# Kernel tuning notes

Measured on AMD Instinct MI355X. Metric: run time of the kernel, lower is better.

## Reference

```python
import jax, jax.numpy as jnp
import numpy as np

KS = 21        # kernel_size
SIGMA = 5.0    # sigma
C = 3          # channels
PAD = KS // 2  # reflection pad = 10


def _gaussian_kernel():
    # Matches torch construction: 2D isotropic Gaussian on integer grid, then
    # normalized to sum 1. Separable => outer product of 1D Gaussians.
    coords = jnp.arange(KS, dtype=jnp.float32)
    mean = (KS - 1) / 2.0
    g1 = jnp.exp(-((coords - mean) ** 2) / (2.0 * SIGMA ** 2))
    k2 = jnp.outer(g1, g1)
    k2 = k2 / jnp.sum(k2)
    # depthwise weight [C, 1, KS, KS] (OIHW with feature_group_count=C)
    return jnp.tile(k2[None, None, :, :], (C, 1, 1, 1))


def setup_inputs() -> dict:
    key = jax.random.key(0)
    x = jax.random.normal(key, (32, 3, 512, 512), dtype=jnp.float32)
    return {"x": x}


def reference(x):
    w = _gaussian_kernel()
    xp = jnp.pad(x, ((0, 0), (0, 0), (PAD, PAD), (PAD, PAD)), mode="reflect")
    out = jax.lax.conv_general_dilated(
        xp, w,
        window_strides=(1, 1),
        padding="VALID",
        dimension_numbers=("NCHW", "OIHW", "NCHW"),
        feature_group_count=C,
    )
    return out  # [B, C, H, W], same spatial size as input
```

## Files before the change

kernel.cpp:

```cpp
#include <hip/hip_runtime.h>
#include <math.h>


#define KS    21
#define PAD   10
#define TILE  64
#define LW    (TILE + 2 * PAD)
#define SKEW  2
#define LWX   88
#define SH    68
#define IMG_H 512
#define IMG_W 512
#define NT    256

__global__ __launch_bounds__(NT) void gauss_blur_kernel(
    const float* __restrict__ in, float* __restrict__ out)
{
    __shared__ __align__(16) float s_in[LW * LWX];
    __shared__ __align__(16) float s_h [LW * SH];

    float w[KS];
    {
        float s = 0.f;
#pragma unroll
        for (int k = 0; k < KS; ++k) {
            float d = (float)(k - PAD);
            w[k] = expf(-d * d * (1.0f / 50.0f));
            s += w[k];
        }
        float inv = 1.0f / s;
#pragma unroll
        for (int k = 0; k < KS; ++k) w[k] *= inv;
    }

    const int tid   = threadIdx.x;
    const int plane = blockIdx.z;
    const int x0    = blockIdx.x * TILE;
    const int y0    = blockIdx.y * TILE;
    const int xbase = x0 - PAD - SKEW;

    const float* __restrict__ pin = in + (size_t)plane * (IMG_H * IMG_W);

    if (xbase >= 0 && xbase + LWX <= IMG_W) {
        for (int idx = tid; idx < LW * (LWX / 4); idx += NT) {
            int ly = idx / (LWX / 4);
            int q  = idx - ly * (LWX / 4);
            int gy = y0 + ly - PAD;
            gy = (gy < 0) ? -gy : ((gy >= IMG_H) ? (2 * IMG_H - 2 - gy) : gy);
            float4 v = *(const float4*)&pin[gy * IMG_W + xbase + 4 * q];
            *(float4*)&s_in[ly * LWX + 4 * q] = v;
        }
    } else {
        for (int idx = tid; idx < LW * LWX; idx += NT) {
            int ly = idx / LWX;
            int j  = idx - ly * LWX;
            int gy = y0 + ly - PAD;
            int gx = xbase + j;
            gy = (gy < 0) ? -gy : ((gy >= IMG_H) ? (2 * IMG_H - 2 - gy) : gy);
            gx = (gx < 0) ? -gx : ((gx >= IMG_W) ? (2 * IMG_W - 2 - gx) : gx);
            s_in[idx] = pin[gy * IMG_W + gx];
        }
    }
    __syncthreads();

    for (int idx = tid; idx < LW * (TILE / 4); idx += NT) {
        int ly = idx >> 4;
        int lx = (idx & 15) << 2;
        const float4* rp = (const float4*)&s_in[ly * LWX + lx];
        float v[28];
#pragma unroll
        for (int t = 0; t < 7; ++t) {
            float4 f = rp[t];
            v[4 * t + 0] = f.x; v[4 * t + 1] = f.y;
            v[4 * t + 2] = f.z; v[4 * t + 3] = f.w;
        }
        float a0 = 0.f, a1 = 0.f, a2 = 0.f, a3 = 0.f;
#pragma unroll
        for (int k = 0; k < KS; ++k) {
            float wk = w[k];
            a0 += wk * v[k + 2];
            a1 += wk * v[k + 3];
            a2 += wk * v[k + 4];
            a3 += wk * v[k + 5];
        }
        *(float4*)&s_h[ly * SH + lx] = make_float4(a0, a1, a2, a3);
    }
    __syncthreads();

    {
        const int c  = tid & 63;
        const int rb = (tid >> 6) << 4;

        float acc[16];
#pragma unroll
        for (int r = 0; r < 16; ++r) acc[r] = 0.f;

#pragma unroll
        for (int t = 0; t < KS + 15; ++t) {
            float v = s_h[(rb + t) * SH + c];
#pragma unroll
            for (int r = 0; r < 16; ++r) {
                int k = t - r;
                if (k >= 0 && k < KS) acc[r] += w[k] * v;
            }
        }

        float* __restrict__ pout = out + (size_t)plane * (IMG_H * IMG_W)
                                       + (size_t)(y0 + rb) * IMG_W + (x0 + c);
#pragma unroll
        for (int r = 0; r < 16; ++r) pout[r * IMG_W] = acc[r];
    }
}

extern "C" void kernel_launch(void* const* d_in, const int* in_sizes, int n_in,
                              void* d_out, int out_size, void* d_ws, size_t ws_size,
                              hipStream_t stream)
{
    const float* x = (const float*)d_in[0];
    float* out = (float*)d_out;

    dim3 grid(IMG_W / TILE, IMG_H / TILE, 96);
    dim3 block(NT);
    gauss_blur_kernel<<<grid, block, 0, stream>>>(x, out);
}
```

Baseline: 226.0 us.

## Read input rows directly from global memory in horizontal pass, drop input LDS tile

Removes the shared-memory staging of the input tile and its barrier. The horizontal pass now loads its 28-element window straight from global memory with float4 reads, falling back to scalar reflected loads on edge tiles. It also adds a min-blocks-per-CU hint of 6 to the launch bounds. Together these cut LDS use and should allow more resident blocks, at the cost of overlapping global reads (seven float4s per thread with heavy overlap), which must now be served by the caches.

```diff
diff --git a/kernel.cpp b/kernel.cpp
--- a/kernel.cpp
+++ b/kernel.cpp
@@ -7,17 +7,15 @@
 #define TILE  64
 #define LW    (TILE + 2 * PAD)
 #define SKEW  2
-#define LWX   88
 #define SH    68
 #define IMG_H 512
 #define IMG_W 512
 #define NT    256
 
-__global__ __launch_bounds__(NT) void gauss_blur_kernel(
+__global__ __launch_bounds__(NT, 6) void gauss_blur_kernel(
     const float* __restrict__ in, float* __restrict__ out)
 {
-    __shared__ __align__(16) float s_in[LW * LWX];
-    __shared__ __align__(16) float s_h [LW * SH];
+    __shared__ __align__(16) float s_h[LW * SH];
 
     float w[KS];
     {
@@ -41,39 +39,34 @@
 
     const float* __restrict__ pin = in + (size_t)plane * (IMG_H * IMG_W);
 
-    if (xbase >= 0 && xbase + LWX <= IMG_W) {
-        for (int idx = tid; idx < LW * (LWX / 4); idx += NT) {
-            int ly = idx / (LWX / 4);
-            int q  = idx - ly * (LWX / 4);
-            int gy = y0 + ly - PAD;
-            gy = (gy < 0) ? -gy : ((gy >= IMG_H) ? (2 * IMG_H - 2 - gy) : gy);
-            float4 v = *(const float4*)&pin[gy * IMG_W + xbase + 4 * q];
-            *(float4*)&s_in[ly * LWX + 4 * q] = v;
-        }
-    } else {
-        for (int idx = tid; idx < LW * LWX; idx += NT) {
-            int ly = idx / LWX;
-            int j  = idx - ly * LWX;
-            int gy = y0 + ly - PAD;
-            int gx = xbase + j;
-            gy = (gy < 0) ? -gy : ((gy >= IMG_H) ? (2 * IMG_H - 2 - gy) : gy);
-            gx = (gx < 0) ? -gx : ((gx >= IMG_W) ? (2 * IMG_W - 2 - gx) : gx);
-            s_in[idx] = pin[gy * IMG_W + gx];
-        }
-    }
-    __syncthreads();
+    const bool xint = (xbase >= 0) && (xbase + 88 <= IMG_W);
 
     for (int idx = tid; idx < LW * (TILE / 4); idx += NT) {
         int ly = idx >> 4;
         int lx = (idx & 15) << 2;
-        const float4* rp = (const float4*)&s_in[ly * LWX + lx];
+        int gy = y0 + ly - PAD;
+        gy = (gy < 0) ? -gy : ((gy >= IMG_H) ? (2 * IMG_H - 2 - gy) : gy);
+        const float* __restrict__ rowp = pin + (size_t)gy * IMG_W;
+
         float v[28];
+        if (xint) {
+            const float4* rp = (const float4*)(rowp + xbase + lx);
 #pragma unroll
-        for (int t = 0; t < 7; ++t) {
-            float4 f = rp[t];
-            v[4 * t + 0] = f.x; v[4 * t + 1] = f.y;
-            v[4 * t + 2] = f.z; v[4 * t + 3] = f.w;
+            for (int t = 0; t < 7; ++t) {
+                float4 f = rp[t];
+                v[4 * t + 0] = f.x; v[4 * t + 1] = f.y;
+                v[4 * t + 2] = f.z; v[4 * t + 3] = f.w;
+            }
+        } else {
+#pragma unroll
+            for (int d = 0; d < 24; ++d) {
+                int gx = xbase + lx + 2 + d;
+                gx = (gx < 0) ? -gx : ((gx >= IMG_W) ? (2 * IMG_W - 2 - gx) : gx);
+                v[d + 2] = rowp[gx];
+            }
+            v[0] = v[1] = v[26] = v[27] = 0.f;
         }
+
         float a0 = 0.f, a1 = 0.f, a2 = 0.f, a3 = 0.f;
 #pragma unroll
         for (int k = 0; k < KS; ++k) {
```

After: 302.2 us. 1.34x slower.
